# Kernel optimization log

Measured on AMD Instinct MI355X. Metric: run time of the kernel, lower is better.

The kernel has to match this reference:

```python
import jax, jax.numpy as jnp
import numpy as np
from itertools import combinations

N_COLS = 16   # number of input features (columns of xl/xu)
ADD = 3       # max subset order
ALPHA = 0.5   # primary compare weight
BETA = 0.8    # tie-break compare weight
BATCH = 65536


def _bitmask(combo):
    m = 0
    for i in combo:
        m |= 1 << i
    return m


def _build_plan(n, add):
    """Static DP plan: for each subset length, gather indices of combo[1:] (left)
    and combo[:-1] (right) among previously computed columns; plus final bitmask order."""
    items = list(range(n))
    index_dict = {(i,): i for i in items}
    count = n
    plan = []
    for length in range(2, min(add, n) + 1):
        combos = list(combinations(items, length))
        if not combos:
            continue
        left = np.array([index_dict[c[1:]] for c in combos], dtype=np.int32)
        right = np.array([index_dict[c[:-1]] for c in combos], dtype=np.int32)
        for c in combos:
            index_dict[c] = count
            count += 1
        plan.append((left, right))
    order = np.array([index_dict[c] for c in sorted(index_dict, key=_bitmask)], dtype=np.int32)
    return plan, order

_PLAN, _ORDER = _build_plan(N_COLS, ADD)


def setup_inputs() -> dict:
    key = jax.random.key(0)
    k1, k2 = jax.random.split(key)
    a = jax.random.uniform(k1, (BATCH, N_COLS), dtype=jnp.float32)
    b = jax.random.uniform(k2, (BATCH, N_COLS), dtype=jnp.float32)
    # valid intervals: xl <= xu elementwise
    xl = jnp.minimum(a, b)
    xu = jnp.maximum(a, b)
    return {"xl": xl, "xu": xu}


def _select_pair(ll, lu, rl, ru):
    # alpha-weighted score; pick the interval with SMALLER score (choose_right when cur > nxt)
    cur = (1.0 - ALPHA) * ll + ALPHA * lu
    nxt = (1.0 - ALPHA) * rl + ALPHA * ru
    # tie-break with beta-weighted score
    beta_cur = (1.0 - BETA) * ll + BETA * lu
    beta_nxt = (1.0 - BETA) * rl + BETA * ru
    choose_right = jnp.where(cur == nxt, beta_cur > beta_nxt, cur > nxt)
    res_l = jnp.where(choose_right, rl, ll)
    res_u = jnp.where(choose_right, ru, lu)
    return res_l, res_u


def reference(xl, xu):
    # mat_* grow by one block per subset length; gathers use static index arrays
    mat_l, mat_u = xl, xu
    for left_idx, right_idx in _PLAN:
        ll = mat_l[:, left_idx]
        lu = mat_u[:, left_idx]
        rl = mat_l[:, right_idx]
        ru = mat_u[:, right_idx]
        res_l, res_u = _select_pair(ll, lu, rl, ru)
        mat_l = jnp.concatenate([mat_l, res_l], axis=1)
        mat_u = jnp.concatenate([mat_u, res_u], axis=1)
    # reorder columns by subset bitmask, as in _reorder_by_bitmask
    return mat_l[:, _ORDER], mat_u[:, _ORDER]
```

## Files before the change

### kernel.cpp

```cpp
#include <hip/hip_runtime.h>
#include <cstdint>

#define NCOLS  696
#define NGROUP 174
#define NREC   136
#define RPB    4
#define BLOCK  256

typedef float v4f __attribute__((ext_vector_type(4)));

constexpr int pr(int a, int b) { return 16 + b * (b - 1) / 2 + a; }

struct alignas(8) RecSrc { uint16_t d[NREC]; };
constexpr RecSrc make_recs() {
    RecSrc t{};
    for (int a = 0; a < 16; ++a) t.d[a] = (uint16_t)(a | (a << 8));
    int p = 16;
    for (int b = 1; b < 16; ++b)
        for (int a = 0; a < b; ++a)
            t.d[p++] = (uint16_t)(a | (b << 8));
    return t;
}

struct alignas(8) ColTbl { uint16_t d[NCOLS]; };
constexpr ColTbl make_cols() {
    ColTbl t{};
    int p = 0;
    for (int h = 0; h < 16; ++h) {
        t.d[p++] = (uint16_t)(h | (h << 8));
        for (int j = 0; j < h; ++j) {
            int pjh = pr(j, h);
            t.d[p++] = (uint16_t)(pjh | (pjh << 8));
            for (int i = 0; i < j; ++i)
                t.d[p++] = (uint16_t)(pr(j, h) | (pr(i, j) << 8));
        }
    }
    return t;
}

__constant__ RecSrc g_recs = make_recs();
__constant__ ColTbl g_cols = make_cols();

__device__ __forceinline__ float2 selpair(float2 L, float2 R) {
    float curL = __fadd_rn(L.x, L.y);
    float curR = __fadd_rn(R.x, R.y);
    float bL = __fadd_rn(__fmul_rn(0.2f, L.x), __fmul_rn(0.8f, L.y));
    float bR = __fadd_rn(__fmul_rn(0.2f, R.x), __fmul_rn(0.8f, R.y));
    bool choose_right = (curL == curR) ? (bL > bR) : (curL > curR);
    return choose_right ? R : L;
}

__device__ __forceinline__ float2 col_compute(const float2* __restrict__ rec,
                                              uint32_t d) {
    float2 L = rec[d & 255u];
    float2 R = rec[(d >> 8) & 255u];
    return selpair(L, R);
}

__global__ __launch_bounds__(BLOCK) void minint_kernel(
    const float* __restrict__ xl, const float* __restrict__ xu,
    float* __restrict__ out, int batch)
{
    __shared__ float2 vals[RPB][16];
    __shared__ float2 recs[RPB][NREC];
    const int t = threadIdx.x;
    const int base = blockIdx.x * RPB;

    if (t < RPB * 16) {
        float a = xl[base * 16 + t];
        float b = xu[base * 16 + t];
        vals[t >> 4][t & 15] = make_float2(a, b);
    }
    __syncthreads();

    const int w    = t >> 6;
    const int lane = t & 63;
    const float2* v = vals[w];

    for (int r = lane; r < NREC; r += 64) {
        uint32_t s = g_recs.d[r];
        float2 lo = v[s & 15u];
        float2 hi = v[(s >> 8) & 15u];
        recs[w][r] = selpair(hi, lo);
    }
    __syncthreads();

    const int row = base + w;
    const float2* rec = recs[w];
    float* outl = out + (size_t)row * NCOLS;
    float* outu = out + (size_t)batch * NCOLS + (size_t)row * NCOLS;
    const ushort4* cols = (const ushort4*)g_cols.d;

    for (int g = lane; g < NGROUP; g += 64) {
        ushort4 d4 = cols[g];
        float2 c0 = col_compute(rec, d4.x);
        float2 c1 = col_compute(rec, d4.y);
        float2 c2 = col_compute(rec, d4.z);
        float2 c3 = col_compute(rec, d4.w);
        v4f rl = { c0.x, c1.x, c2.x, c3.x };
        v4f ru = { c0.y, c1.y, c2.y, c3.y };
        __builtin_nontemporal_store(rl, (v4f*)(outl + 4 * g));
        __builtin_nontemporal_store(ru, (v4f*)(outu + 4 * g));
    }
}

extern "C" void kernel_launch(void* const* d_in, const int* in_sizes, int n_in,
                              void* d_out, int out_size, void* d_ws, size_t ws_size,
                              hipStream_t stream) {
    const float* xl = (const float*)d_in[0];
    const float* xu = (const float*)d_in[1];
    float* out = (float*)d_out;
    const int batch = in_sizes[0] / 16;
    const int grid  = batch / RPB;
    minint_kernel<<<grid, BLOCK, 0, stream>>>(xl, xu, out, batch);
}
```

Baseline: 374.6 us.

## Process several rows per wave with a fixed grid and drop block barriers

Each wave now loops over eight consecutive rows and uses its own shared-memory slice, so the block-wide __syncthreads calls are gone. The launch uses a fixed grid of 2048 blocks instead of one block per four rows. The aim is to cut block launch and barrier overhead and keep waves streaming output stores. The trade-off is that each row's input load sits serially on the wave's critical path with no prefetch. The hardcoded grid only covers a batch of up to 65536 rows, and correctness relies on LDS operations within a wave completing in order.

Result: slower. 403.3 us (+7.7%).

```diff
diff --git a/kernel.cpp b/kernel.cpp
--- a/kernel.cpp
+++ b/kernel.cpp
@@ -4,8 +4,10 @@
 #define NCOLS  696
 #define NGROUP 174
 #define NREC   136
-#define RPB    4
+#define WPB    4
 #define BLOCK  256
+#define GRID   2048
+#define ROWS_PER_WAVE 8
 
 typedef float v4f __attribute__((ext_vector_type(4)));
 
@@ -61,46 +63,56 @@
     const float* __restrict__ xl, const float* __restrict__ xu,
     float* __restrict__ out, int batch)
 {
-    __shared__ float2 vals[RPB][16];
-    __shared__ float2 recs[RPB][NREC];
-    const int t = threadIdx.x;
-    const int base = blockIdx.x * RPB;
-
-    if (t < RPB * 16) {
-        float a = xl[base * 16 + t];
-        float b = xu[base * 16 + t];
-        vals[t >> 4][t & 15] = make_float2(a, b);
-    }
-    __syncthreads();
-
+    __shared__ float2 vals[WPB][16];
+    __shared__ float2 recs[WPB][NREC];
+    const int t    = threadIdx.x;
     const int w    = t >> 6;
     const int lane = t & 63;
-    const float2* v = vals[w];
+    const int wgid = blockIdx.x * WPB + w;
 
-    for (int r = lane; r < NREC; r += 64) {
-        uint32_t s = g_recs.d[r];
-        float2 lo = v[s & 15u];
-        float2 hi = v[(s >> 8) & 15u];
-        recs[w][r] = selpair(hi, lo);
-    }
-    __syncthreads();
-
-    const int row = base + w;
-    const float2* rec = recs[w];
-    float* outl = out + (size_t)row * NCOLS;
-    float* outu = out + (size_t)batch * NCOLS + (size_t)row * NCOLS;
+    float2* v   = vals[w];
+    float2* rec = recs[w];
     const ushort4* cols = (const ushort4*)g_cols.d;
 
-    for (int g = lane; g < NGROUP; g += 64) {
-        ushort4 d4 = cols[g];
-        float2 c0 = col_compute(rec, d4.x);
-        float2 c1 = col_compute(rec, d4.y);
-        float2 c2 = col_compute(rec, d4.z);
-        float2 c3 = col_compute(rec, d4.w);
-        v4f rl = { c0.x, c1.x, c2.x, c3.x };
-        v4f ru = { c0.y, c1.y, c2.y, c3.y };
-        __builtin_nontemporal_store(rl, (v4f*)(outl + 4 * g));
-        __builtin_nontemporal_store(ru, (v4f*)(outu + 4 * g));
+    for (int it = 0; it < ROWS_PER_WAVE; ++it) {
+        const int row = wgid * ROWS_PER_WAVE + it;
+        if (row >= batch) break;
+
+        if (lane < 32) {
+            const float* src = (lane < 16) ? (xl + (size_t)row * 16 + lane)
+                                           : (xu + (size_t)row * 16 + (lane - 16));
+            ((float*)v)[(lane & 15) * 2 + (lane >> 4)] = *src;
+        }
+
+        #pragma unroll
+        for (int m = 0; m < 3; ++m) {
+            int r = lane + 64 * m;
+            if (r < NREC) {
+                uint32_t s = g_recs.d[r];
+                float2 lo = v[s & 15u];
+                float2 hi = v[(s >> 8) & 15u];
+                rec[r] = selpair(hi, lo);
+            }
+        }
+
+        float* outl = out + (size_t)row * NCOLS;
+        float* outu = out + (size_t)batch * NCOLS + (size_t)row * NCOLS;
+
+        #pragma unroll
+        for (int k = 0; k < 3; ++k) {
+            int g = lane + 64 * k;
+            if (g < NGROUP) {
+                ushort4 d4 = cols[g];
+                float2 c0 = col_compute(rec, d4.x);
+                float2 c1 = col_compute(rec, d4.y);
+                float2 c2 = col_compute(rec, d4.z);
+                float2 c3 = col_compute(rec, d4.w);
+                v4f rl = { c0.x, c1.x, c2.x, c3.x };
+                v4f ru = { c0.y, c1.y, c2.y, c3.y };
+                __builtin_nontemporal_store(rl, (v4f*)(outl + 4 * g));
+                __builtin_nontemporal_store(ru, (v4f*)(outu + 4 * g));
+            }
+        }
     }
 }
 
@@ -111,6 +123,5 @@
     const float* xu = (const float*)d_in[1];
     float* out = (float*)d_out;
     const int batch = in_sizes[0] / 16;
-    const int grid  = batch / RPB;
-    minint_kernel<<<grid, BLOCK, 0, stream>>>(xl, xu, out, batch);
+    minint_kernel<<<GRID, BLOCK, 0, stream>>>(xl, xu, out, batch);
 }
```
